# Performance work log

Hardware: AMD Instinct MI355X
Metric: run time of the kernel (lower is better)

The kernel has to match this reference:

```python
import jax, jax.numpy as jnp
import numpy as np

B, T, C = 256, 512, 128


def setup_inputs() -> dict:
    key = jax.random.key(0)
    k1, k2, k3 = jax.random.split(key, 3)
    inputs = jax.random.normal(k1, (B, T, C), dtype=jnp.float32)
    # learned transition matrix (orthogonal init approximated by scaled normal)
    transitions = jax.random.normal(k2, (C, C), dtype=jnp.float32) * 0.1
    # variable sequence lengths in [T//2, T] -> keras-style boolean mask
    lengths = jax.random.randint(k3, (B,), T // 2, T + 1)
    mask = jnp.arange(T)[None, :] < lengths[:, None]  # [B, T] bool
    return {"inputs": inputs, "mask": mask, "transitions": transitions}


def reference(inputs, mask, transitions):
    # Faithful port of CRF.call: sequence_lengths from mask, then Viterbi decode
    # (tfa.text.crf_decode): max-plus forward DP with backpointers + backtrack.
    Bn, Tn, Cn = inputs.shape
    seq_len = jnp.sum(mask.astype(jnp.int32), axis=-1)  # [B]

    ident = jnp.arange(Cn, dtype=jnp.int32)[None, :]  # identity backpointer row

    def fwd_step(state, xs):
        # state: [B, C] best score ending in each tag
        pot_t, valid = xs  # [B, C], [B] bool
        scores = state[:, :, None] + transitions[None]      # [B, Cprev, Ccur]
        new_state = jnp.max(scores, axis=1) + pot_t          # [B, C]
        bp = jnp.argmax(scores, axis=1).astype(jnp.int32)    # [B, C]
        state = jnp.where(valid[:, None], new_state, state)  # carry past length
        bp = jnp.where(valid[:, None], bp, ident)            # identity beyond length
        return state, bp

    pots = jnp.swapaxes(inputs[:, 1:], 0, 1)  # [T-1, B, C]
    valid = mask[:, 1:].T                      # [T-1, B]
    state, bps = jax.lax.scan(fwd_step, inputs[:, 0], (pots, valid))

    last_tag = jnp.argmax(state, axis=-1).astype(jnp.int32)  # [B]

    def bwd_step(tag, bp_t):
        prev = jnp.take_along_axis(bp_t, tag[:, None], axis=1)[:, 0]
        return prev, prev

    _, tags_rest = jax.lax.scan(bwd_step, last_tag, bps, reverse=True)  # [T-1, B]
    viterbi = jnp.concatenate([tags_rest, last_tag[None]], axis=0).T    # [B, T]
    return viterbi, inputs, seq_len, transitions
```

## Files before the change

kernel.cpp:

```cpp
#include <hip/hip_runtime.h>


#define BB 256
#define TT 512
#define CC 128
#define NTH 1024
#define GR 8
#define JP 16
#define SPAD 20

#define OFF_VIT 0
#define OFF_INP (BB * TT)
#define OFF_LEN (OFF_INP + BB * TT * CC)
#define OFF_TR (OFF_LEN + BB)

#define BP_BYTES ((TT - 1) * CC)
#define STATE_FLOATS (2 * GR * SPAD)
#define SMEM_BYTES (BP_BYTES + STATE_FLOATS * 4 + 16 * 4 + 16)

#define F3(a, b, c) fmaxf(fmaxf((a), (b)), (c))

template <int C>
__device__ __forceinline__ float dppmaxf(float v) {
  float o = __int_as_float(__builtin_amdgcn_update_dpp(0, __float_as_int(v), C, 0xF, 0xF, true));
  return fmaxf(v, o);
}
template <int C>
__device__ __forceinline__ unsigned dppminu(unsigned v) {
  unsigned o = (unsigned)__builtin_amdgcn_update_dpp(0, (int)v, C, 0xF, 0xF, true);
  return v < o ? v : o;
}

__device__ __forceinline__ void lexmax(float& v, int& i, float ov, int oi) {
  bool take = (ov > v) || (ov == v && oi < i);
  v = take ? ov : v;
  i = take ? oi : i;
}
template <int C>
__device__ __forceinline__ void bfly_dpp(float& v, int& i) {
  float ov = __int_as_float(__builtin_amdgcn_update_dpp(0, __float_as_int(v), C, 0xF, 0xF, true));
  int oi = __builtin_amdgcn_update_dpp(0, i, C, 0xF, 0xF, true);
  lexmax(v, i, ov, oi);
}
__device__ __forceinline__ void bfly6(float& v, int& i) {
  bfly_dpp<0xB1>(v, i);
  bfly_dpp<0x4E>(v, i);
  bfly_dpp<0x141>(v, i);
  bfly_dpp<0x140>(v, i);
  { float ov = __shfl_xor(v, 16); int oi = __shfl_xor(i, 16); lexmax(v, i, ov, oi); }
  { float ov = __shfl_xor(v, 32); int oi = __shfl_xor(i, 32); lexmax(v, i, ov, oi); }
}

#define DO_BP                                                                  \
  {                                                                            \
    unsigned iA = 255u, iB = 255u;                                             \
    iA = (s7 == sm) ? 7u : iA;  iB = (sF == sm) ? 15u : iB;                    \
    iA = (s6 == sm) ? 6u : iA;  iB = (sE == sm) ? 14u : iB;                    \
    iA = (s5 == sm) ? 5u : iA;  iB = (sD == sm) ? 13u : iB;                    \
    iA = (s4 == sm) ? 4u : iA;  iB = (sC == sm) ? 12u : iB;                    \
    iA = (s3 == sm) ? 3u : iA;  iB = (sB == sm) ? 11u : iB;                    \
    iA = (s2 == sm) ? 2u : iA;  iB = (sA == sm) ? 10u : iB;                    \
    iA = (s1 == sm) ? 1u : iA;  iB = (s9 == sm) ? 9u : iB;                     \
    iA = (s0 == sm) ? 0u : iA;  iB = (s8 == sm) ? 8u : iB;                     \
    unsigned bi = ((iA != 255u) ? iA : iB) + gbase;                            \
    bi = dppminu<0xB1>(bi);                                                    \
    bi = dppminu<0x4E>(bi);                                                    \
    bi = dppminu<0x141>(bi);                                                   \
    if (g0) *bpw = (unsigned char)bi;                                          \
    bpw += CC;                                                                 \
  }

#define STEP(ROFF, WOFF, SH)                                                   \
  {                                                                            \
    const float4* rp_ = (const float4*)(state_s + (ROFF) + g * SPAD);          \
    float4 a0 = rp_[0], a1 = rp_[1], a2 = rp_[2], a3 = rp_[3];                 \
    float potB = 0.f;                                                          \
    if (g0) potB = prow2[ccur];                                                \
    prow2 = (prow2 < prowLast) ? prow2 + CC : prow2;                           \
    if (SH) DO_BP                                                              \
    float t0 = a0.x + tr[0], t1 = a0.y + tr[1], t2 = a0.z + tr[2],             \
          t3 = a0.w + tr[3];                                                   \
    float t4 = a1.x + tr[4], t5 = a1.y + tr[5], t6 = a1.z + tr[6],             \
          t7 = a1.w + tr[7];                                                   \
    float t8 = a2.x + tr[8], t9 = a2.y + tr[9], tA = a2.z + tr[10],            \
          tB = a2.w + tr[11];                                                  \
    float tC = a3.x + tr[12], tD = a3.y + tr[13], tE = a3.z + tr[14],          \
          tF = a3.w + tr[15];                                                  \
    float m = fmaxf(F3(F3(t0, t1, t2), F3(t3, t4, t5), F3(t6, t7, t8)),        \
                    F3(F3(t9, tA, tB), F3(tC, tD, tE), tF));                   \
    m = dppmaxf<0xB1>(m);                                                      \
    m = dppmaxf<0x4E>(m);                                                      \
    m = dppmaxf<0x141>(m);                                                     \
    if (g0) *(state_s + (WOFF) + wslot) = m + pot;                             \
    pot = potA; potA = potB;                                                   \
    s0 = t0; s1 = t1; s2 = t2; s3 = t3; s4 = t4; s5 = t5; s6 = t6; s7 = t7;    \
    s8 = t8; s9 = t9; sA = tA; sB = tB; sC = tC; sD = tD; sE = tE; sF = tF;    \
    sm = m;                                                                    \
    asm volatile("s_waitcnt lgkmcnt(0)\n\ts_barrier" ::: "memory");            \
  }

__global__ __launch_bounds__(NTH, 1) void crf_viterbi(
    const float* __restrict__ inputs, const unsigned char* __restrict__ mask_bytes,
    const float* __restrict__ trans, float* __restrict__ out) {
  extern __shared__ unsigned char smem[];
  unsigned char* bp_s = smem;
  float* state_s = (float*)(smem + BP_BYTES);
  int* wsum = (int*)(state_s + STATE_FLOATS);

  const int b = blockIdx.x;
  const int tid = threadIdx.x;
  const int lane = tid & 63;
  const int wave = tid >> 6;
  const int ccur = tid >> 3;
  const int g = tid & 7;
  const bool g0 = (g == 0);
  const unsigned gbase = (unsigned)(g * JP);
  const int wslot = (ccur >> 4) * SPAD + (ccur & 15);

  const int w4 = (mask_bytes[1] == 0) ? 4 : 1;
  if (tid < TT) {
    int mb = mask_bytes[(size_t)(b * TT + tid) * (size_t)w4] != 0;
    unsigned long long bal = __ballot(mb);
    if (lane == 0) wsum[wave] = __popcll(bal);
  }

  float tr[JP];
#pragma unroll
  for (int j = 0; j < JP; ++j) tr[j] = trans[(g * JP + j) * CC + ccur];

  const float* pin = inputs + (size_t)b * TT * CC;

  if (tid < CC) state_s[(tid >> 4) * SPAD + (tid & 15)] = pin[tid];
  __syncthreads();

  int L = 0;
#pragma unroll
  for (int i = 0; i < 8; ++i) L += wsum[i];

  float pot = 0.f, potA = 0.f;
  if (g0) {
    pot = pin[CC + ccur];
    potA = pin[2 * CC + ccur];
  }
  const float* prow2 = pin + 3 * CC;
  const float* prowLast = pin + (size_t)(L - 1) * CC;

  float s0, s1, s2, s3, s4, s5, s6, s7, s8, s9, sA, sB, sC, sD, sE, sF, sm;
  unsigned char* bpw = bp_s + ccur;

  STEP(0, GR * SPAD, 0);
  int t = 2;
  for (; t + 1 < L; t += 2) {
    STEP(GR * SPAD, 0, 1);
    STEP(0, GR * SPAD, 1);
  }
  if (t < L) {
    STEP(GR * SPAD, 0, 1);
  }
  DO_BP
  asm volatile("s_waitcnt lgkmcnt(0)\n\ts_barrier" ::: "memory");

  float* outv = out + OFF_VIT + b * TT;

  if (wave == 0) {
    const float* fs = state_s + ((L - 1) & 1) * (GR * SPAD);
    float v1 = fs[(lane >> 4) * SPAD + (lane & 15)];
    int c2 = lane + 64;
    float v2 = fs[(c2 >> 4) * SPAD + (c2 & 15)];
    float v;
    int idx;
    if (v2 > v1) { v = v2; idx = c2; } else { v = v1; idx = lane; }
    bfly6(v, idx);

    for (int t2 = L - 1 + lane; t2 < TT; t2 += 64) outv[t2] = (float)idx;
    if (lane == 0) {
      out[OFF_LEN + b] = (float)L;
      int cur = idx;
      for (int tt = L - 2; tt >= 0; --tt) {
        cur = bp_s[tt * CC + cur];
        outv[tt] = (float)cur;
      }
    }
  } else {
    if (wave == 1) out[OFF_TR + b * 64 + lane] = trans[b * 64 + lane];
    const float4* src = (const float4*)pin;
    float4* dst = (float4*)(out + OFF_INP + (size_t)b * TT * CC);
    for (int i = tid - 64; i < TT * CC / 4; i += NTH - 64) dst[i] = src[i];
  }
}

extern "C" void kernel_launch(void* const* d_in, const int* in_sizes, int n_in,
                              void* d_out, int out_size, void* d_ws, size_t ws_size,
                              hipStream_t stream) {
  const float* inputs = (const float*)d_in[0];
  const unsigned char* mask = (const unsigned char*)d_in[1];
  const float* trans = (const float*)d_in[2];
  float* out = (float*)d_out;

  crf_viterbi<<<BB, NTH, SMEM_BYTES, stream>>>(inputs, mask, trans, out);
}
```

Baseline: 411.0 us.

## Halve threads per tag, use packed f32 adds, overlap input copy with DP

Each current tag is now handled by 4 threads of 32 previous tags instead of 8 threads of 16, so the block shrinks to 512 threads and the cross-lane max and argmin need one fewer DPP step. The transition adds use v_pk_add_f32 on float pairs. The passthrough copy of the inputs is spread across the loop iterations of the serial forward DP, with any remainder copied after it, instead of being done in one pass at the end. The trade-off is more serial work per thread on the critical path and more register pressure, in exchange for shorter reductions and barriers across fewer waves.

```diff
diff --git a/kernel.cpp b/kernel.cpp
--- a/kernel.cpp
+++ b/kernel.cpp
@@ -4,10 +4,10 @@
 #define BB 256
 #define TT 512
 #define CC 128
-#define NTH 1024
-#define GR 8
-#define JP 16
-#define SPAD 20
+#define NTH 512
+#define GR 4
+#define JP 32
+#define SPAD 40
 
 #define OFF_VIT 0
 #define OFF_INP (BB * TT)
@@ -18,6 +18,18 @@
 #define STATE_FLOATS (2 * GR * SPAD)
 #define SMEM_BYTES (BP_BYTES + STATE_FLOATS * 4 + 16 * 4 + 16)
 
+#define SIDX(c) ((((c) >> 5) * SPAD) + ((c) & 31))
+
+typedef float v2f __attribute__((ext_vector_type(2)));
+
+__device__ __forceinline__ v2f pkadd(v2f a, v2f b) {
+  v2f d;
+  asm("v_pk_add_f32 %0, %1, %2" : "=v"(d) : "v"(a), "v"(b));
+  return d;
+}
+__device__ __forceinline__ v2f lo4(float4 q) { return (v2f){q.x, q.y}; }
+__device__ __forceinline__ v2f hi4(float4 q) { return (v2f){q.z, q.w}; }
+
 #define F3(a, b, c) fmaxf(fmaxf((a), (b)), (c))
 
 template <int C>
@@ -30,6 +42,7 @@
   unsigned o = (unsigned)__builtin_amdgcn_update_dpp(0, (int)v, C, 0xF, 0xF, true);
   return v < o ? v : o;
 }
+__device__ __forceinline__ unsigned uminu(unsigned a, unsigned b) { return a < b ? a : b; }
 
 __device__ __forceinline__ void lexmax(float& v, int& i, float ov, int oi) {
   bool take = (ov > v) || (ov == v && oi < i);
@@ -51,52 +64,62 @@
   { float ov = __shfl_xor(v, 32); int oi = __shfl_xor(i, 32); lexmax(v, i, ov, oi); }
 }
 
-#define DO_BP                                                                  \
-  {                                                                            \
-    unsigned iA = 255u, iB = 255u;                                             \
-    iA = (s7 == sm) ? 7u : iA;  iB = (sF == sm) ? 15u : iB;                    \
-    iA = (s6 == sm) ? 6u : iA;  iB = (sE == sm) ? 14u : iB;                    \
-    iA = (s5 == sm) ? 5u : iA;  iB = (sD == sm) ? 13u : iB;                    \
-    iA = (s4 == sm) ? 4u : iA;  iB = (sC == sm) ? 12u : iB;                    \
-    iA = (s3 == sm) ? 3u : iA;  iB = (sB == sm) ? 11u : iB;                    \
-    iA = (s2 == sm) ? 2u : iA;  iB = (sA == sm) ? 10u : iB;                    \
-    iA = (s1 == sm) ? 1u : iA;  iB = (s9 == sm) ? 9u : iB;                     \
-    iA = (s0 == sm) ? 0u : iA;  iB = (s8 == sm) ? 8u : iB;                     \
-    unsigned bi = ((iA != 255u) ? iA : iB) + gbase;                            \
-    bi = dppminu<0xB1>(bi);                                                    \
-    bi = dppminu<0x4E>(bi);                                                    \
-    bi = dppminu<0x141>(bi);                                                   \
-    if (g0) *bpw = (unsigned char)bi;                                          \
-    bpw += CC;                                                                 \
-  }
-
-#define STEP(ROFF, WOFF, SH)                                                   \
-  {                                                                            \
-    const float4* rp_ = (const float4*)(state_s + (ROFF) + g * SPAD);          \
-    float4 a0 = rp_[0], a1 = rp_[1], a2 = rp_[2], a3 = rp_[3];                 \
-    float potB = 0.f;                                                          \
-    if (g0) potB = prow2[ccur];                                                \
-    prow2 = (prow2 < prowLast) ? prow2 + CC : prow2;                           \
-    if (SH) DO_BP                                                              \
-    float t0 = a0.x + tr[0], t1 = a0.y + tr[1], t2 = a0.z + tr[2],             \
-          t3 = a0.w + tr[3];                                                   \
-    float t4 = a1.x + tr[4], t5 = a1.y + tr[5], t6 = a1.z + tr[6],             \
-          t7 = a1.w + tr[7];                                                   \
-    float t8 = a2.x + tr[8], t9 = a2.y + tr[9], tA = a2.z + tr[10],            \
-          tB = a2.w + tr[11];                                                  \
-    float tC = a3.x + tr[12], tD = a3.y + tr[13], tE = a3.z + tr[14],          \
-          tF = a3.w + tr[15];                                                  \
-    float m = fmaxf(F3(F3(t0, t1, t2), F3(t3, t4, t5), F3(t6, t7, t8)),        \
-                    F3(F3(t9, tA, tB), F3(tC, tD, tE), tF));                   \
-    m = dppmaxf<0xB1>(m);                                                      \
-    m = dppmaxf<0x4E>(m);                                                      \
-    m = dppmaxf<0x141>(m);                                                     \
-    if (g0) *(state_s + (WOFF) + wslot) = m + pot;                             \
-    pot = potA; potA = potB;                                                   \
-    s0 = t0; s1 = t1; s2 = t2; s3 = t3; s4 = t4; s5 = t5; s6 = t6; s7 = t7;    \
-    s8 = t8; s9 = t9; sA = tA; sB = tB; sC = tC; sD = tD; sE = tE; sF = tF;    \
-    sm = m;                                                                    \
-    asm volatile("s_waitcnt lgkmcnt(0)\n\ts_barrier" ::: "memory");            \
+#define DO_BP                                                                   \
+  {                                                                             \
+    unsigned iA = 255u, iB = 255u, iC = 255u, iD = 255u;                        \
+    iA = (sp3.y == sm) ? 7u : iA;   iB = (sp7.y == sm) ? 15u : iB;              \
+    iA = (sp3.x == sm) ? 6u : iA;   iB = (sp7.x == sm) ? 14u : iB;              \
+    iA = (sp2.y == sm) ? 5u : iA;   iB = (sp6.y == sm) ? 13u : iB;              \
+    iA = (sp2.x == sm) ? 4u : iA;   iB = (sp6.x == sm) ? 12u : iB;              \
+    iA = (sp1.y == sm) ? 3u : iA;   iB = (sp5.y == sm) ? 11u : iB;              \
+    iA = (sp1.x == sm) ? 2u : iA;   iB = (sp5.x == sm) ? 10u : iB;              \
+    iA = (sp0.y == sm) ? 1u : iA;   iB = (sp4.y == sm) ? 9u : iB;               \
+    iA = (sp0.x == sm) ? 0u : iA;   iB = (sp4.x == sm) ? 8u : iB;               \
+    iC = (spB.y == sm) ? 23u : iC;  iD = (spF.y == sm) ? 31u : iD;              \
+    iC = (spB.x == sm) ? 22u : iC;  iD = (spF.x == sm) ? 30u : iD;              \
+    iC = (spA.y == sm) ? 21u : iC;  iD = (spE.y == sm) ? 29u : iD;              \
+    iC = (spA.x == sm) ? 20u : iC;  iD = (spE.x == sm) ? 28u : iD;              \
+    iC = (sp9.y == sm) ? 19u : iC;  iD = (spD.y == sm) ? 27u : iD;              \
+    iC = (sp9.x == sm) ? 18u : iC;  iD = (spD.x == sm) ? 26u : iD;              \
+    iC = (sp8.y == sm) ? 17u : iC;  iD = (spC.y == sm) ? 25u : iD;              \
+    iC = (sp8.x == sm) ? 16u : iC;  iD = (spC.x == sm) ? 24u : iD;              \
+    unsigned bi = uminu(uminu(iA, iB), uminu(iC, iD)) + gbase;                  \
+    bi = dppminu<0xB1>(bi);                                                     \
+    bi = dppminu<0x4E>(bi);                                                     \
+    if (g0) *bpw = (unsigned char)bi;                                           \
+    bpw += CC;                                                                  \
+  }
+
+#define STEP(ROFF, WOFF, SH)                                                    \
+  {                                                                             \
+    const float4* rp_ = (const float4*)(state_s + (ROFF) + g * SPAD);           \
+    float4 a0 = rp_[0], a1 = rp_[1], a2 = rp_[2], a3 = rp_[3];                  \
+    float4 a4 = rp_[4], a5 = rp_[5], a6 = rp_[6], a7 = rp_[7];                  \
+    float potB = 0.f;                                                           \
+    if (g0) potB = rowp[ccur];                                                  \
+    rowp = (rowp < rowLast) ? rowp + CC : rowp;                                 \
+    if (SH) DO_BP                                                               \
+    v2f p0 = pkadd(lo4(a0), trp[0]), p1 = pkadd(hi4(a0), trp[1]);               \
+    v2f p2 = pkadd(lo4(a1), trp[2]), p3 = pkadd(hi4(a1), trp[3]);               \
+    v2f p4 = pkadd(lo4(a2), trp[4]), p5 = pkadd(hi4(a2), trp[5]);               \
+    v2f p6 = pkadd(lo4(a3), trp[6]), p7 = pkadd(hi4(a3), trp[7]);               \
+    v2f p8 = pkadd(lo4(a4), trp[8]), p9 = pkadd(hi4(a4), trp[9]);               \
+    v2f pA = pkadd(lo4(a5), trp[10]), pB = pkadd(hi4(a5), trp[11]);             \
+    v2f pC = pkadd(lo4(a6), trp[12]), pD = pkadd(hi4(a6), trp[13]);             \
+    v2f pE = pkadd(lo4(a7), trp[14]), pF = pkadd(hi4(a7), trp[15]);             \
+    float m = fmaxf(                                                            \
+        F3(F3(F3(p0.x, p0.y, p1.x), F3(p1.y, p2.x, p2.y), F3(p3.x, p3.y, p4.x)),\
+           F3(F3(p4.y, p5.x, p5.y), F3(p6.x, p6.y, p7.x), F3(p7.y, p8.x, p8.y)),\
+           F3(F3(p9.x, p9.y, pA.x), F3(pA.y, pB.x, pB.y), F3(pC.x, pC.y, pD.x))),\
+        F3(fmaxf(pD.y, pE.x), fmaxf(pE.y, pF.x), pF.y));                        \
+    m = dppmaxf<0xB1>(m);                                                       \
+    m = dppmaxf<0x4E>(m);                                                       \
+    if (g0) *(state_s + (WOFF) + wslot) = m + pot;                              \
+    pot = potA; potA = potB;                                                    \
+    sp0 = p0; sp1 = p1; sp2 = p2; sp3 = p3; sp4 = p4; sp5 = p5; sp6 = p6;       \
+    sp7 = p7; sp8 = p8; sp9 = p9; spA = pA; spB = pB; spC = pC; spD = pD;       \
+    spE = pE; spF = pF; sm = m;                                                 \
+    asm volatile("s_waitcnt lgkmcnt(0)\n\ts_barrier" ::: "memory");             \
   }
 
 __global__ __launch_bounds__(NTH, 1) void crf_viterbi(
@@ -111,26 +134,29 @@
   const int tid = threadIdx.x;
   const int lane = tid & 63;
   const int wave = tid >> 6;
-  const int ccur = tid >> 3;
-  const int g = tid & 7;
+  const int ccur = tid >> 2;
+  const int g = tid & 3;
   const bool g0 = (g == 0);
   const unsigned gbase = (unsigned)(g * JP);
-  const int wslot = (ccur >> 4) * SPAD + (ccur & 15);
+  const int wslot = SIDX(ccur);
 
   const int w4 = (mask_bytes[1] == 0) ? 4 : 1;
-  if (tid < TT) {
+  {
     int mb = mask_bytes[(size_t)(b * TT + tid) * (size_t)w4] != 0;
     unsigned long long bal = __ballot(mb);
     if (lane == 0) wsum[wave] = __popcll(bal);
   }
 
-  float tr[JP];
+  v2f trp[16];
 #pragma unroll
-  for (int j = 0; j < JP; ++j) tr[j] = trans[(g * JP + j) * CC + ccur];
+  for (int k = 0; k < 16; ++k) {
+    trp[k].x = trans[(g * JP + 2 * k) * CC + ccur];
+    trp[k].y = trans[(g * JP + 2 * k + 1) * CC + ccur];
+  }
 
   const float* pin = inputs + (size_t)b * TT * CC;
 
-  if (tid < CC) state_s[(tid >> 4) * SPAD + (tid & 15)] = pin[tid];
+  if (tid < CC) state_s[SIDX(tid)] = pin[tid];
   __syncthreads();
 
   int L = 0;
@@ -142,31 +168,40 @@
     pot = pin[CC + ccur];
     potA = pin[2 * CC + ccur];
   }
-  const float* prow2 = pin + 3 * CC;
-  const float* prowLast = pin + (size_t)(L - 1) * CC;
-
-  float s0, s1, s2, s3, s4, s5, s6, s7, s8, s9, sA, sB, sC, sD, sE, sF, sm;
+  const float* rowp = pin + 3 * CC;
+  const float* rowLast = pin + (size_t)(TT - 1) * CC;
+
+  v2f sp0{}, sp1{}, sp2{}, sp3{}, sp4{}, sp5{}, sp6{}, sp7{};
+  v2f sp8{}, sp9{}, spA{}, spB{}, spC{}, spD{}, spE{}, spF{};
+  float sm = 0.f;
   unsigned char* bpw = bp_s + ccur;
+
+  const float4* src4 = (const float4*)pin;
+  float4* dst4 = (float4*)(out + OFF_INP + (size_t)b * TT * CC);
+  int cp = 0;
+  float4 cpv{};
 
   STEP(0, GR * SPAD, 0);
   int t = 2;
   for (; t + 1 < L; t += 2) {
     STEP(GR * SPAD, 0, 1);
+    if (cp < 32) cpv = src4[cp * NTH + tid];
     STEP(0, GR * SPAD, 1);
-  }
-  if (t < L) {
-    STEP(GR * SPAD, 0, 1);
-  }
+    if (cp < 32) { dst4[cp * NTH + tid] = cpv; ++cp; }
+  }
+  if (t < L) STEP(GR * SPAD, 0, 1);
   DO_BP
   asm volatile("s_waitcnt lgkmcnt(0)\n\ts_barrier" ::: "memory");
 
+  for (; cp < 32; ++cp) dst4[cp * NTH + tid] = src4[cp * NTH + tid];
+
   float* outv = out + OFF_VIT + b * TT;
 
   if (wave == 0) {
     const float* fs = state_s + ((L - 1) & 1) * (GR * SPAD);
-    float v1 = fs[(lane >> 4) * SPAD + (lane & 15)];
+    float v1 = fs[SIDX(lane)];
     int c2 = lane + 64;
-    float v2 = fs[(c2 >> 4) * SPAD + (c2 & 15)];
+    float v2 = fs[SIDX(c2)];
     float v;
     int idx;
     if (v2 > v1) { v = v2; idx = c2; } else { v = v1; idx = lane; }
@@ -181,11 +216,8 @@
         outv[tt] = (float)cur;
       }
     }
-  } else {
-    if (wave == 1) out[OFF_TR + b * 64 + lane] = trans[b * 64 + lane];
-    const float4* src = (const float4*)pin;
-    float4* dst = (float4*)(out + OFF_INP + (size_t)b * TT * CC);
-    for (int i = tid - 64; i < TT * CC / 4; i += NTH - 64) dst[i] = src[i];
+  } else if (wave == 1) {
+    out[OFF_TR + b * 64 + lane] = trans[b * 64 + lane];
   }
 }
 
```

New measurement: 439.2 us. 1.07x slower.
